# Optimization experiments

Hardware: AMD Instinct MI355X
Metric: run time of the kernel (lower is better)

The kernel has to match this reference:

```python
import jax, jax.numpy as jnp
import numpy as np

NB_HEAD = 8
SIZE_PER_HEAD = 64
MAX_LEN = 1024
D_IN = 512
BATCH = 8
NEG_BIG = 1e12  # matches the torch module's mask * 1000000000000.0


def setup_inputs() -> dict:
    key = jax.random.key(0)
    ks = jax.random.split(key, 6)
    return {
        "Q_seq": jax.random.normal(ks[0], (BATCH, MAX_LEN, D_IN), dtype=jnp.float32),
        "K_seq": jax.random.normal(ks[1], (BATCH, MAX_LEN, D_IN), dtype=jnp.float32),
        "V_seq": jax.random.normal(ks[2], (BATCH, MAX_LEN, D_IN), dtype=jnp.float32),
        "WQ": jax.random.normal(ks[3], (D_IN, NB_HEAD * SIZE_PER_HEAD), dtype=jnp.float32),
        "WK": jax.random.normal(ks[4], (D_IN, NB_HEAD * SIZE_PER_HEAD), dtype=jnp.float32),
        "WV": jax.random.normal(ks[5], (D_IN, NB_HEAD * SIZE_PER_HEAD), dtype=jnp.float32),
    }


def reference(Q_seq, K_seq, V_seq, WQ, WK, WV):
    B, L, _ = Q_seq.shape
    H, D = NB_HEAD, SIZE_PER_HEAD
    # QKV projections -> [B, H, L, D]
    q = (Q_seq @ WQ).reshape(B, L, H, D).transpose(0, 2, 1, 3)
    k = (K_seq @ WK).reshape(B, L, H, D).transpose(0, 2, 1, 3)
    v = (V_seq @ WV).reshape(B, L, H, D).transpose(0, 2, 1, 3)
    # scaled dot-product scores [B, H, Lq, Lk]
    scores = jnp.einsum("bhqd,bhkd->bhqk", q, k) / jnp.sqrt(jnp.float32(D))
    # causal mask: the torch Mask() subtracts 1e12 where key_idx > query_idx
    causal = jnp.triu(jnp.ones((L, L), dtype=scores.dtype), k=1)  # 1 where k > q
    scores = scores - causal[None, None, :, :] * NEG_BIG
    attn = jax.nn.softmax(scores, axis=-1)
    out = jnp.einsum("bhqk,bhkd->bhqd", attn, v)  # [B, H, L, D]
    return out.transpose(0, 2, 1, 3).reshape(B, L, H * D)
```

## Files before the change

### kernel.cpp

```cpp
#include <hip/hip_runtime.h>
#include <cstddef>

#define LEN    1024
#define DIN    512
#define NHEAD  8
#define HDIM   64
#define BATCH  8

typedef __attribute__((ext_vector_type(8))) short  short8;
typedef __attribute__((ext_vector_type(4))) float  f32x4;

#define MFMA16(a, b, c) __builtin_amdgcn_mfma_f32_16x16x32_bf16((a), (b), (c), 0, 0, 0)
#define PERM_HI 0x07060302u
#define PERM_LO 0x05040100u

__device__ __forceinline__ unsigned short bf_hi(float x) {
    unsigned u = __float_as_uint(x);
    return (unsigned short)((u + 0x7fffu + ((u >> 16) & 1u)) >> 16);
}
__device__ __forceinline__ void bf_split(float x, unsigned short& h, unsigned short& l) {
    unsigned u  = __float_as_uint(x);
    unsigned hu = (u + 0x7fffu + ((u >> 16) & 1u)) >> 16;
    h = (unsigned short)hu;
    l = bf_hi(x - __uint_as_float(hu << 16));
}
__device__ __forceinline__ void unpack4(uint4 u, ushort4& h, ushort4& l) {
    h = make_ushort4((unsigned short)(u.x >> 16), (unsigned short)(u.y >> 16),
                     (unsigned short)(u.z >> 16), (unsigned short)(u.w >> 16));
    l = make_ushort4((unsigned short)(u.x & 0xffff), (unsigned short)(u.y & 0xffff),
                     (unsigned short)(u.z & 0xffff), (unsigned short)(u.w & 0xffff));
}
__device__ __forceinline__ void unpack8(uint4 a, uint4 b, uint4& h, uint4& l) {
    h = make_uint4(__builtin_amdgcn_perm(a.y, a.x, PERM_HI),
                   __builtin_amdgcn_perm(a.w, a.z, PERM_HI),
                   __builtin_amdgcn_perm(b.y, b.x, PERM_HI),
                   __builtin_amdgcn_perm(b.w, b.z, PERM_HI));
    l = make_uint4(__builtin_amdgcn_perm(a.y, a.x, PERM_LO),
                   __builtin_amdgcn_perm(a.w, a.z, PERM_LO),
                   __builtin_amdgcn_perm(b.y, b.x, PERM_LO),
                   __builtin_amdgcn_perm(b.w, b.z, PERM_LO));
}

template<int CTRL>
__device__ __forceinline__ float dpp_mov(float x) {
    return __int_as_float(__builtin_amdgcn_update_dpp(
        0, __float_as_int(x), CTRL, 0xF, 0xF, true));
}
__device__ __forceinline__ float red16_max(float x) {
    x = fmaxf(x, dpp_mov<0xB1>(x));
    x = fmaxf(x, dpp_mov<0x4E>(x));
    x = fmaxf(x, dpp_mov<0x141>(x));
    x = fmaxf(x, dpp_mov<0x140>(x));
    return x;
}
__device__ __forceinline__ float red16_sum(float x) {
    x += dpp_mov<0xB1>(x);
    x += dpp_mov<0x4E>(x);
    x += dpp_mov<0x141>(x);
    x += dpp_mov<0x140>(x);
    return x;
}

__global__ __launch_bounds__(256)
void wprep(const float* __restrict__ WQ, const float* __restrict__ WK,
           const float* __restrict__ WV, unsigned short* __restrict__ wt)
{
    __shared__ float T[64][68];
    const int z = blockIdx.z;
    const float* W = (z == 0) ? WQ : (z == 1) ? WK : WV;
    unsigned short* Wth = wt + (size_t)z * 524288;
    unsigned short* Wtl = Wth + 262144;
    const int k0 = blockIdx.x * 64, n0 = blockIdx.y * 64;
    const int t = threadIdx.x;
    #pragma unroll
    for (int e = 0; e < 4; ++e) {
        int f = e * 256 + t, r = f >> 4, c4 = (f & 15) << 2;
        *(float4*)&T[r][c4] = *(const float4*)&W[(size_t)(k0 + r) * 512 + n0 + c4];
    }
    __syncthreads();
    #pragma unroll
    for (int e = 0; e < 4; ++e) {
        int f = e * 256 + t, nr = f >> 4, kc4 = (f & 15) << 2;
        ushort4 h, l;
        bf_split(T[kc4 + 0][nr], h.x, l.x);
        bf_split(T[kc4 + 1][nr], h.y, l.y);
        bf_split(T[kc4 + 2][nr], h.z, l.z);
        bf_split(T[kc4 + 3][nr], h.w, l.w);
        *(ushort4*)&Wth[(size_t)(n0 + nr) * 512 + k0 + kc4] = h;
        *(ushort4*)&Wtl[(size_t)(n0 + nr) * 512 + k0 + kc4] = l;
    }
}

#define PSTR 40

__global__ __launch_bounds__(256, 3)
void proj_mfma(const float* __restrict__ Qin, const float* __restrict__ Kin,
               const float* __restrict__ Vin, const unsigned short* __restrict__ wt,
               unsigned int* __restrict__ qhl, unsigned int* __restrict__ khl,
               unsigned short* __restrict__ vh)
{
    __shared__ unsigned short Ah[128 * PSTR], Al[128 * PSTR],
                              Bh[128 * PSTR], Bl[128 * PSTR];
    const int z = blockIdx.z;
    const bool full = (z < 2);
    const float* X = (z == 0) ? Qin : (z == 1) ? Kin : Vin;
    const unsigned short* Wth = wt + (size_t)z * 524288;
    const unsigned short* Wtl = Wth + 262144;

    const int t = threadIdx.x, lane = t & 63, w = t >> 6;
    const int wm = w & 1, wn = w >> 1;
    const int m0 = blockIdx.x * 128, n0 = blockIdx.y * 128;
    const int lm = lane & 15, lq = lane >> 4;
    const int ar = t >> 1, ak = (t & 1) * 16;

    const float* Xp = X + (size_t)(m0 + ar) * 512 + ak;
    const unsigned short* Bph = Wth + (size_t)(n0 + ar) * 512 + ak;
    const unsigned short* Bpl = Wtl + (size_t)(n0 + ar) * 512 + ak;

    f32x4 acc[4][4];
    #pragma unroll
    for (int i = 0; i < 4; ++i)
        #pragma unroll
        for (int j = 0; j < 4; ++j) acc[i][j] = 0.f;

    float4 av[4];
    uint4 bh0, bh1, bl0, bl1;
    #pragma unroll
    for (int e = 0; e < 4; ++e) av[e] = *(const float4*)(Xp + e * 4);
    bh0 = *(const uint4*)(Bph);
    bh1 = *(const uint4*)(Bph + 8);
    if (full) { bl0 = *(const uint4*)(Bpl); bl1 = *(const uint4*)(Bpl + 8); }

    for (int k0 = 0; k0 < 512; k0 += 32) {
        __syncthreads();
        {
            const float* ff = (const float*)&av[0];
            uint hw[16];
            #pragma unroll
            for (int i = 0; i < 16; ++i) hw[i] = __float_as_uint(ff[i]) & 0xffff0000u;
            uint4 ahv  = make_uint4(__builtin_amdgcn_perm(hw[1],  hw[0],  PERM_HI),
                                    __builtin_amdgcn_perm(hw[3],  hw[2],  PERM_HI),
                                    __builtin_amdgcn_perm(hw[5],  hw[4],  PERM_HI),
                                    __builtin_amdgcn_perm(hw[7],  hw[6],  PERM_HI));
            uint4 ahv2 = make_uint4(__builtin_amdgcn_perm(hw[9],  hw[8],  PERM_HI),
                                    __builtin_amdgcn_perm(hw[11], hw[10], PERM_HI),
                                    __builtin_amdgcn_perm(hw[13], hw[12], PERM_HI),
                                    __builtin_amdgcn_perm(hw[15], hw[14], PERM_HI));
            *(uint4*)&Ah[ar * PSTR + ak]     = ahv;
            *(uint4*)&Ah[ar * PSTR + ak + 8] = ahv2;
            if (full) {
                uint lo[8];
                #pragma unroll
                for (int i = 0; i < 8; ++i) {
                    float r0 = ff[2*i]   - __uint_as_float(hw[2*i]);
                    float r1 = ff[2*i+1] - __uint_as_float(hw[2*i+1]);
                    lo[i] = ((uint)bf_hi(r1) << 16) | bf_hi(r0);
                }
                *(uint4*)&Al[ar * PSTR + ak]     = make_uint4(lo[0], lo[1], lo[2], lo[3]);
                *(uint4*)&Al[ar * PSTR + ak + 8] = make_uint4(lo[4], lo[5], lo[6], lo[7]);
            }
        }
        *(uint4*)&Bh[ar * PSTR + ak]     = bh0;
        *(uint4*)&Bh[ar * PSTR + ak + 8] = bh1;
        if (full) {
            *(uint4*)&Bl[ar * PSTR + ak]     = bl0;
            *(uint4*)&Bl[ar * PSTR + ak + 8] = bl1;
        }
        __syncthreads();

        if (k0 + 32 < 512) {
            #pragma unroll
            for (int e = 0; e < 4; ++e) av[e] = *(const float4*)(Xp + k0 + 32 + e * 4);
            bh0 = *(const uint4*)(Bph + k0 + 32);
            bh1 = *(const uint4*)(Bph + k0 + 40);
            if (full) {
                bl0 = *(const uint4*)(Bpl + k0 + 32);
                bl1 = *(const uint4*)(Bpl + k0 + 40);
            }
        }

        short8 a_h[4], a_l[4];
        #pragma unroll
        for (int mi = 0; mi < 4; ++mi) {
            int off = (wm * 64 + mi * 16 + lm) * PSTR + lq * 8;
            a_h[mi] = *(const short8*)&Ah[off];
            if (full) a_l[mi] = *(const short8*)&Al[off];
        }
        #pragma unroll
        for (int ni = 0; ni < 4; ++ni) {
            int off = (wn * 64 + ni * 16 + lm) * PSTR + lq * 8;
            short8 b_h = *(const short8*)&Bh[off];
            if (full) {
                short8 b_l = *(const short8*)&Bl[off];
                #pragma unroll
                for (int mi = 0; mi < 4; ++mi) {
                    acc[mi][ni] = MFMA16(a_l[mi], b_h, acc[mi][ni]);
                    acc[mi][ni] = MFMA16(a_h[mi], b_l, acc[mi][ni]);
                    acc[mi][ni] = MFMA16(a_h[mi], b_h, acc[mi][ni]);
                }
            } else {
                #pragma unroll
                for (int mi = 0; mi < 4; ++mi)
                    acc[mi][ni] = MFMA16(a_h[mi], b_h, acc[mi][ni]);
            }
        }
    }

    if (z < 2) {
        unsigned int* o = (z == 0) ? qhl : khl;
        const float sc = (z == 0) ? 0.18033688011112042f : 1.0f;
        #pragma unroll
        for (int mi = 0; mi < 4; ++mi)
            #pragma unroll
            for (int ni = 0; ni < 4; ++ni) {
                int n_abs = n0 + wn * 64 + ni * 16 + lm;
                int hd = n_abs >> 6, d = n_abs & 63;
                #pragma unroll
                for (int r = 0; r < 4; ++r) {
                    int m_abs = m0 + wm * 64 + mi * 16 + lq * 4 + r;
                    int b = m_abs >> 10, li = m_abs & 1023;
                    unsigned short hv, lv;
                    bf_split(acc[mi][ni][r] * sc, hv, lv);
                    o[(((size_t)b * NHEAD + hd) * LEN + li) * HDIM + d] =
                        ((unsigned)hv << 16) | lv;
                }
            }
    } else {
        #pragma unroll
        for (int mi = 0; mi < 4; ++mi) {
            int m_base = m0 + wm * 64 + mi * 16 + lq * 4;
            int b = m_base >> 10, l0 = m_base & 1023;
            #pragma unroll
            for (int ni = 0; ni < 4; ++ni) {
                int n_abs = n0 + wn * 64 + ni * 16 + lm;
                int hd = n_abs >> 6, d = n_abs & 63;
                ushort4 hv = make_ushort4(bf_hi(acc[mi][ni][0]), bf_hi(acc[mi][ni][1]),
                                          bf_hi(acc[mi][ni][2]), bf_hi(acc[mi][ni][3]));
                *(ushort4*)&vh[(((size_t)b * NHEAD + hd) * HDIM + d) * LEN + l0] = hv;
            }
        }
    }
}

__global__ __launch_bounds__(256)
void attn_mfma(const unsigned int* __restrict__ qhl, const unsigned int* __restrict__ khl,
               const unsigned short* __restrict__ vth, float* __restrict__ out)
{
    __shared__ unsigned short sm[18432];
    unsigned short* Kh  = sm;
    unsigned short* Kl  = sm + 4608;
    unsigned short* Pb  = sm;
    unsigned short* Vt  = sm + 9728;
    unsigned short* Qsh = sm;
    unsigned short* Qsl = sm + 9216;

    const int t = threadIdx.x, lane = t & 63, w = t >> 6;
    const int lm = lane & 15, lq = lane >> 4;
    const int bx = blockIdx.x;
    const int bh = bx & 63;
    const int g  = (bx >> 6) & 3;
    const int qt = (((bx >> 8) ^ bx) & 1) ? (7 - g) : g;
    const size_t base = (size_t)bh * LEN * HDIM;
    const unsigned int*   qb = qhl + base;
    const unsigned int*   kb = khl + base;
    const unsigned short* vb = vth + base;
    const int Q0  = qt * 128;
    const int Q0w = Q0 + w * 32;

    #pragma unroll
    for (int e = 0; e < 8; ++e) {
        int f = e * 256 + t, r = f >> 4, c4 = (f & 15) << 2;
        uint4 u = *(const uint4*)&qb[(size_t)(Q0 + r) * 64 + c4];
        ushort4 h, l;
        unpack4(u, h, l);
        *(ushort4*)&Qsh[r * 72 + c4] = h;
        *(ushort4*)&Qsl[r * 72 + c4] = l;
    }
    __syncthreads();
    short8 qfh[2][2], qfl[2][2];
    #pragma unroll
    for (int mi = 0; mi < 2; ++mi)
        #pragma unroll
        for (int ks = 0; ks < 2; ++ks) {
            int off = (w * 32 + mi * 16 + lm) * 72 + ks * 32 + lq * 8;
            qfh[mi][ks] = *(const short8*)&Qsh[off];
            qfl[mi][ks] = *(const short8*)&Qsl[off];
        }

    float m_i[2][4], l_i[2][4];
    f32x4 oacc[2][4];
    #pragma unroll
    for (int mi = 0; mi < 2; ++mi)
        #pragma unroll
        for (int r = 0; r < 4; ++r) { m_i[mi][r] = -1e30f; l_i[mi][r] = 0.f; }
    #pragma unroll
    for (int mi = 0; mi < 2; ++mi)
        #pragma unroll
        for (int nd = 0; nd < 4; ++nd) oacc[mi][nd] = 0.f;

    const int kr = t >> 2, kq = t & 3;
    const int vd_ = t >> 3, vs8 = (t & 7) << 3;

    uint4 kreg[4], vreg[2];
    #pragma unroll
    for (int e = 0; e < 4; ++e)
        kreg[e] = *(const uint4*)&kb[(size_t)kr * 64 + kq * 16 + e * 4];
    #pragma unroll
    for (int e = 0; e < 2; ++e)
        vreg[e] = *(const uint4*)&vb[(size_t)(e * 32 + vd_) * LEN + vs8];

    const int jend = 2 * qt + 1;
    for (int jb = 0; jb <= jend; ++jb) {
        __syncthreads();
        {
            uint4 h0, l0, h1, l1;
            unpack8(kreg[0], kreg[1], h0, l0);
            unpack8(kreg[2], kreg[3], h1, l1);
            int ko = kr * 72 + kq * 16;
            *(uint4*)&Kh[ko]     = h0;
            *(uint4*)&Kh[ko + 8] = h1;
            *(uint4*)&Kl[ko]     = l0;
            *(uint4*)&Kl[ko + 8] = l1;
            *(uint4*)&Vt[(vd_)      * 72 + vs8] = vreg[0];
            *(uint4*)&Vt[(vd_ + 32) * 72 + vs8] = vreg[1];
        }
        __syncthreads();

        if (jb < jend) {
            #pragma unroll
            for (int e = 0; e < 4; ++e)
                kreg[e] = *(const uint4*)&kb[(size_t)((jb + 1) * 64 + kr) * 64 + kq * 16 + e * 4];
            #pragma unroll
            for (int e = 0; e < 2; ++e)
                vreg[e] = *(const uint4*)&vb[(size_t)(e * 32 + vd_) * LEN + (jb + 1) * 64 + vs8];
        }

        const bool active = (jb * 64 <= Q0w + 31);
        f32x4 sf[2][4];
        if (active) {
            #pragma unroll
            for (int mi = 0; mi < 2; ++mi)
                #pragma unroll
                for (int ni = 0; ni < 4; ++ni) sf[mi][ni] = 0.f;
            #pragma unroll
            for (int ks = 0; ks < 2; ++ks)
                #pragma unroll
                for (int ni = 0; ni < 4; ++ni) {
                    int off = (ni * 16 + lm) * 72 + ks * 32 + lq * 8;
                    short8 b_h = *(const short8*)&Kh[off];
                    short8 b_l = *(const short8*)&Kl[off];
                    #pragma unroll
                    for (int mi = 0; mi < 2; ++mi) {
                        sf[mi][ni] = MFMA16(qfl[mi][ks], b_h, sf[mi][ni]);
                        sf[mi][ni] = MFMA16(qfh[mi][ks], b_l, sf[mi][ni]);
                        sf[mi][ni] = MFMA16(qfh[mi][ks], b_h, sf[mi][ni]);
                    }
                }
            if (jb * 64 + 63 > Q0w) {
                #pragma unroll
                for (int mi = 0; mi < 2; ++mi)
                    #pragma unroll
                    for (int ni = 0; ni < 4; ++ni) {
                        int key = jb * 64 + ni * 16 + lm;
                        #pragma unroll
                        for (int r = 0; r < 4; ++r) {
                            int qi = Q0w + mi * 16 + lq * 4 + r;
                            if (key > qi) sf[mi][ni][r] = -1e30f;
                        }
                    }
            }
        }
        __syncthreads();

        if (active) {
            #pragma unroll
            for (int mi = 0; mi < 2; ++mi)
                #pragma unroll
                for (int r = 0; r < 4; ++r) {
                    float mv = fmaxf(fmaxf(sf[mi][0][r], sf[mi][1][r]),
                                     fmaxf(sf[mi][2][r], sf[mi][3][r]));
                    mv = red16_max(mv);
                    float mo = m_i[mi][r];
                    float mn = fmaxf(mo, mv);
                    float al = __builtin_amdgcn_exp2f(mo - mn);
                    m_i[mi][r] = mn;
                    float rs = 0.f;
                    int prow = (w * 32 + mi * 16 + lq * 4 + r) * 76 + lm;
                    #pragma unroll
                    for (int ni = 0; ni < 4; ++ni) {
                        float p = __builtin_amdgcn_exp2f(sf[mi][ni][r] - mn);
                        rs += p;
                        Pb[prow + ni * 16] = bf_hi(p);
                    }
                    rs = red16_sum(rs);
                    l_i[mi][r] = l_i[mi][r] * al + rs;
                    #pragma unroll
                    for (int nd = 0; nd < 4; ++nd) oacc[mi][nd][r] *= al;
                }
            short8 pf[2][2];
            #pragma unroll
            for (int mi = 0; mi < 2; ++mi)
                #pragma unroll
                for (int ks = 0; ks < 2; ++ks)
                    pf[mi][ks] = *(const short8*)&Pb[(w * 32 + mi * 16 + lm) * 76 + ks * 32 + lq * 8];
            #pragma unroll
            for (int ks = 0; ks < 2; ++ks)
                #pragma unroll
                for (int nd = 0; nd < 4; ++nd) {
                    short8 vf = *(const short8*)&Vt[(nd * 16 + lm) * 72 + ks * 32 + lq * 8];
                    #pragma unroll
                    for (int mi = 0; mi < 2; ++mi)
                        oacc[mi][nd] = MFMA16(pf[mi][ks], vf, oacc[mi][nd]);
                }
        }
    }

    const int b = bh >> 3, hd = bh & 7;
    #pragma unroll
    for (int mi = 0; mi < 2; ++mi)
        #pragma unroll
        for (int r = 0; r < 4; ++r) {
            int qrow = Q0w + mi * 16 + lq * 4 + r;
            float inv = 1.0f / l_i[mi][r];
            #pragma unroll
            for (int nd = 0; nd < 4; ++nd) {
                int d = nd * 16 + lm;
                out[((size_t)b * LEN + qrow) * (NHEAD * HDIM) + hd * 64 + d] =
                    oacc[mi][nd][r] * inv;
            }
        }
}

extern "C" void kernel_launch(void* const* d_in, const int* in_sizes, int n_in,
                              void* d_out, int out_size, void* d_ws, size_t ws_size,
                              hipStream_t stream)
{
    const float* Qin = (const float*)d_in[0];
    const float* Kin = (const float*)d_in[1];
    const float* Vin = (const float*)d_in[2];
    const float* WQ  = (const float*)d_in[3];
    const float* WK  = (const float*)d_in[4];
    const float* WV  = (const float*)d_in[5];

    const size_t per = (size_t)BATCH * NHEAD * LEN * HDIM;
    unsigned int*   qhl = (unsigned int*)d_ws;
    unsigned int*   khl = qhl + per;
    unsigned short* vh  = (unsigned short*)(khl + per);
    unsigned short* wt  = vh + per;

    wprep    <<<dim3(8, 8, 3),  256, 0, stream>>>(WQ, WK, WV, wt);
    proj_mfma<<<dim3(64, 4, 3), 256, 0, stream>>>(Qin, Kin, Vin, wt, qhl, khl, vh);
    attn_mfma<<<dim3(512),      256, 0, stream>>>(qhl, khl, vh, (float*)d_out);
}
```

Baseline: 188.2 us.

## Widen attention key tile from 64 to 128 and drop per-warp activity gating

Doubles the key/value tile processed per loop iteration in the attention kernel from 64 to 128 keys. This halves the number of iterations and barriers, and loads twice as much K/V per thread per step. The per-warp 'active' skip is removed, so warps whose queries lie entirely before part of the final tile now compute and mask extra scores. Shared memory grows to hold the larger K, V and P tiles, which may lower occupancy.

```diff
diff --git a/kernel.cpp b/kernel.cpp
--- a/kernel.cpp
+++ b/kernel.cpp
@@ -246,11 +246,11 @@
 void attn_mfma(const unsigned int* __restrict__ qhl, const unsigned int* __restrict__ khl,
                const unsigned short* __restrict__ vth, float* __restrict__ out)
 {
-    __shared__ unsigned short sm[18432];
+    __shared__ __align__(16) unsigned short sm[27136];
     unsigned short* Kh  = sm;
-    unsigned short* Kl  = sm + 4608;
+    unsigned short* Kl  = sm + 9216;
     unsigned short* Pb  = sm;
-    unsigned short* Vt  = sm + 9728;
+    unsigned short* Vt  = sm + 18432;
     unsigned short* Qsh = sm;
     unsigned short* Qsl = sm + 9216;
 
@@ -298,120 +298,126 @@
         #pragma unroll
         for (int nd = 0; nd < 4; ++nd) oacc[mi][nd] = 0.f;
 
-    const int kr = t >> 2, kq = t & 3;
-    const int vd_ = t >> 3, vs8 = (t & 7) << 3;
-
-    uint4 kreg[4], vreg[2];
-    #pragma unroll
-    for (int e = 0; e < 4; ++e)
-        kreg[e] = *(const uint4*)&kb[(size_t)kr * 64 + kq * 16 + e * 4];
+    const int kr = t >> 1, kq = t & 1;
+    const int vd_ = t >> 3, vs16 = (t & 7) << 4;
+
+    uint4 kreg[8], vreg[4];
+    #pragma unroll
+    for (int e = 0; e < 8; ++e)
+        kreg[e] = *(const uint4*)&kb[(size_t)kr * 64 + kq * 32 + e * 4];
     #pragma unroll
     for (int e = 0; e < 2; ++e)
-        vreg[e] = *(const uint4*)&vb[(size_t)(e * 32 + vd_) * LEN + vs8];
-
-    const int jend = 2 * qt + 1;
+        #pragma unroll
+        for (int u = 0; u < 2; ++u)
+            vreg[e * 2 + u] = *(const uint4*)&vb[(size_t)(e * 32 + vd_) * LEN + vs16 + u * 8];
+
+    const int jend = qt;
     for (int jb = 0; jb <= jend; ++jb) {
         __syncthreads();
         {
-            uint4 h0, l0, h1, l1;
+            uint4 h0, l0, h1, l1, h2, l2, h3, l3;
             unpack8(kreg[0], kreg[1], h0, l0);
             unpack8(kreg[2], kreg[3], h1, l1);
-            int ko = kr * 72 + kq * 16;
-            *(uint4*)&Kh[ko]     = h0;
-            *(uint4*)&Kh[ko + 8] = h1;
-            *(uint4*)&Kl[ko]     = l0;
-            *(uint4*)&Kl[ko + 8] = l1;
-            *(uint4*)&Vt[(vd_)      * 72 + vs8] = vreg[0];
-            *(uint4*)&Vt[(vd_ + 32) * 72 + vs8] = vreg[1];
+            unpack8(kreg[4], kreg[5], h2, l2);
+            unpack8(kreg[6], kreg[7], h3, l3);
+            int ko = kr * 72 + kq * 32;
+            *(uint4*)&Kh[ko]      = h0;
+            *(uint4*)&Kh[ko + 8]  = h1;
+            *(uint4*)&Kh[ko + 16] = h2;
+            *(uint4*)&Kh[ko + 24] = h3;
+            *(uint4*)&Kl[ko]      = l0;
+            *(uint4*)&Kl[ko + 8]  = l1;
+            *(uint4*)&Kl[ko + 16] = l2;
+            *(uint4*)&Kl[ko + 24] = l3;
+            int vo = vd_ * 136 + vs16;
+            *(uint4*)&Vt[vo]              = vreg[0];
+            *(uint4*)&Vt[vo + 8]          = vreg[1];
+            *(uint4*)&Vt[vo + 32 * 136]     = vreg[2];
+            *(uint4*)&Vt[vo + 32 * 136 + 8] = vreg[3];
         }
         __syncthreads();
 
         if (jb < jend) {
             #pragma unroll
-            for (int e = 0; e < 4; ++e)
-                kreg[e] = *(const uint4*)&kb[(size_t)((jb + 1) * 64 + kr) * 64 + kq * 16 + e * 4];
+            for (int e = 0; e < 8; ++e)
+                kreg[e] = *(const uint4*)&kb[(size_t)((jb + 1) * 128 + kr) * 64 + kq * 32 + e * 4];
             #pragma unroll
             for (int e = 0; e < 2; ++e)
-                vreg[e] = *(const uint4*)&vb[(size_t)(e * 32 + vd_) * LEN + (jb + 1) * 64 + vs8];
-        }
-
-        const bool active = (jb * 64 <= Q0w + 31);
-        f32x4 sf[2][4];
-        if (active) {
+                #pragma unroll
+                for (int u = 0; u < 2; ++u)
+                    vreg[e * 2 + u] = *(const uint4*)&vb[(size_t)(e * 32 + vd_) * LEN + (jb + 1) * 128 + vs16 + u * 8];
+        }
+
+        f32x4 sf[2][8];
+        #pragma unroll
+        for (int mi = 0; mi < 2; ++mi)
+            #pragma unroll
+            for (int ni = 0; ni < 8; ++ni) sf[mi][ni] = 0.f;
+        #pragma unroll
+        for (int ks = 0; ks < 2; ++ks)
+            #pragma unroll
+            for (int ni = 0; ni < 8; ++ni) {
+                int off = (ni * 16 + lm) * 72 + ks * 32 + lq * 8;
+                short8 b_h = *(const short8*)&Kh[off];
+                short8 b_l = *(const short8*)&Kl[off];
+                #pragma unroll
+                for (int mi = 0; mi < 2; ++mi) {
+                    sf[mi][ni] = MFMA16(qfl[mi][ks], b_h, sf[mi][ni]);
+                    sf[mi][ni] = MFMA16(qfh[mi][ks], b_l, sf[mi][ni]);
+                    sf[mi][ni] = MFMA16(qfh[mi][ks], b_h, sf[mi][ni]);
+                }
+            }
+        if (jb == jend) {
             #pragma unroll
             for (int mi = 0; mi < 2; ++mi)
                 #pragma unroll
-                for (int ni = 0; ni < 4; ++ni) sf[mi][ni] = 0.f;
-            #pragma unroll
-            for (int ks = 0; ks < 2; ++ks)
-                #pragma unroll
-                for (int ni = 0; ni < 4; ++ni) {
-                    int off = (ni * 16 + lm) * 72 + ks * 32 + lq * 8;
-                    short8 b_h = *(const short8*)&Kh[off];
-                    short8 b_l = *(const short8*)&Kl[off];
+                for (int ni = 0; ni < 8; ++ni) {
+                    int key = jb * 128 + ni * 16 + lm;
                     #pragma unroll
-                    for (int mi = 0; mi < 2; ++mi) {
-                        sf[mi][ni] = MFMA16(qfl[mi][ks], b_h, sf[mi][ni]);
-                        sf[mi][ni] = MFMA16(qfh[mi][ks], b_l, sf[mi][ni]);
-                        sf[mi][ni] = MFMA16(qfh[mi][ks], b_h, sf[mi][ni]);
+                    for (int r = 0; r < 4; ++r) {
+                        int qi = Q0w + mi * 16 + lq * 4 + r;
+                        if (key > qi) sf[mi][ni][r] = -1e30f;
                     }
                 }
-            if (jb * 64 + 63 > Q0w) {
-                #pragma unroll
-                for (int mi = 0; mi < 2; ++mi)
-                    #pragma unroll
-                    for (int ni = 0; ni < 4; ++ni) {
-                        int key = jb * 64 + ni * 16 + lm;
-                        #pragma unroll
-                        for (int r = 0; r < 4; ++r) {
-                            int qi = Q0w + mi * 16 + lq * 4 + r;
-                            if (key > qi) sf[mi][ni][r] = -1e30f;
-                        }
-                    }
-            }
         }
         __syncthreads();
 
-        if (active) {
-            #pragma unroll
-            for (int mi = 0; mi < 2; ++mi)
-                #pragma unroll
-                for (int r = 0; r < 4; ++r) {
-                    float mv = fmaxf(fmaxf(sf[mi][0][r], sf[mi][1][r]),
-                                     fmaxf(sf[mi][2][r], sf[mi][3][r]));
-                    mv = red16_max(mv);
-                    float mo = m_i[mi][r];
-                    float mn = fmaxf(mo, mv);
-                    float al = __builtin_amdgcn_exp2f(mo - mn);
-                    m_i[mi][r] = mn;
-                    float rs = 0.f;
-                    int prow = (w * 32 + mi * 16 + lq * 4 + r) * 76 + lm;
-                    #pragma unroll
-                    for (int ni = 0; ni < 4; ++ni) {
-                        float p = __builtin_amdgcn_exp2f(sf[mi][ni][r] - mn);
-                        rs += p;
-                        Pb[prow + ni * 16] = bf_hi(p);
-                    }
-                    rs = red16_sum(rs);
-                    l_i[mi][r] = l_i[mi][r] * al + rs;
-                    #pragma unroll
-                    for (int nd = 0; nd < 4; ++nd) oacc[mi][nd][r] *= al;
-                }
-            short8 pf[2][2];
-            #pragma unroll
-            for (int mi = 0; mi < 2; ++mi)
-                #pragma unroll
-                for (int ks = 0; ks < 2; ++ks)
-                    pf[mi][ks] = *(const short8*)&Pb[(w * 32 + mi * 16 + lm) * 76 + ks * 32 + lq * 8];
-            #pragma unroll
-            for (int ks = 0; ks < 2; ++ks)
-                #pragma unroll
-                for (int nd = 0; nd < 4; ++nd) {
-                    short8 vf = *(const short8*)&Vt[(nd * 16 + lm) * 72 + ks * 32 + lq * 8];
-                    #pragma unroll
-                    for (int mi = 0; mi < 2; ++mi)
-                        oacc[mi][nd] = MFMA16(pf[mi][ks], vf, oacc[mi][nd]);
-                }
+        #pragma unroll
+        for (int mi = 0; mi < 2; ++mi)
+            #pragma unroll
+            for (int r = 0; r < 4; ++r) {
+                float mv = fmaxf(fmaxf(fmaxf(sf[mi][0][r], sf[mi][1][r]),
+                                       fmaxf(sf[mi][2][r], sf[mi][3][r])),
+                                 fmaxf(fmaxf(sf[mi][4][r], sf[mi][5][r]),
+                                       fmaxf(sf[mi][6][r], sf[mi][7][r])));
+                mv = red16_max(mv);
+                float mo = m_i[mi][r];
+                float mn = fmaxf(mo, mv);
+                float al = __builtin_amdgcn_exp2f(mo - mn);
+                m_i[mi][r] = mn;
+                float rs = 0.f;
+                int prow = (w * 32 + mi * 16 + lq * 4 + r) * 132 + lm;
+                #pragma unroll
+                for (int ni = 0; ni < 8; ++ni) {
+                    float p = __builtin_amdgcn_exp2f(sf[mi][ni][r] - mn);
+                    rs += p;
+                    Pb[prow + ni * 16] = bf_hi(p);
+                }
+                rs = red16_sum(rs);
+                l_i[mi][r] = l_i[mi][r] * al + rs;
+                #pragma unroll
+                for (int nd = 0; nd < 4; ++nd) oacc[mi][nd][r] *= al;
+            }
+        #pragma unroll
+        for (int ks = 0; ks < 4; ++ks) {
+            short8 pf0 = *(const short8*)&Pb[(w * 32 + 0  + lm) * 132 + ks * 32 + lq * 8];
+            short8 pf1 = *(const short8*)&Pb[(w * 32 + 16 + lm) * 132 + ks * 32 + lq * 8];
+            #pragma unroll
+            for (int nd = 0; nd < 4; ++nd) {
+                short8 vf = *(const short8*)&Vt[(nd * 16 + lm) * 136 + ks * 32 + lq * 8];
+                oacc[0][nd] = MFMA16(pf0, vf, oacc[0][nd]);
+                oacc[1][nd] = MFMA16(pf1, vf, oacc[1][nd]);
+            }
         }
     }
 
```

New measurement: 204.6 us. +8.7%, slower.

## Split attention KV range across two blocks and merge with a combine kernel

Applied to the files above, without the earlier changes.

The attention kernel now splits each query tile's key/value blocks into even and odd halves, so 1024 blocks run instead of 512. Each block writes unnormalized partial outputs plus running max and sum to workspace, and a new combine kernel merges the two halves and normalizes. The goal is more parallelism to fill the GPU's CUs, and it drops the previous causal load-balancing remap. The cost is an extra kernel launch and a round trip of partial results through global memory. The combine step uses exp2 on the stored max values, which assumes the partial kernel keeps m in log2 scale.

```diff
diff --git a/kernel.cpp b/kernel.cpp
--- a/kernel.cpp
+++ b/kernel.cpp
@@ -242,9 +242,10 @@
     }
 }
 
-__global__ __launch_bounds__(256)
-void attn_mfma(const unsigned int* __restrict__ qhl, const unsigned int* __restrict__ khl,
-               const unsigned short* __restrict__ vth, float* __restrict__ out)
+__global__ __launch_bounds__(256, 4)
+void attn_part(const unsigned int* __restrict__ qhl, const unsigned int* __restrict__ khl,
+               const unsigned short* __restrict__ vth,
+               float* __restrict__ opart, float* __restrict__ mlpart)
 {
     __shared__ unsigned short sm[18432];
     unsigned short* Kh  = sm;
@@ -258,8 +259,8 @@
     const int lm = lane & 15, lq = lane >> 4;
     const int bx = blockIdx.x;
     const int bh = bx & 63;
-    const int g  = (bx >> 6) & 3;
-    const int qt = (((bx >> 8) ^ bx) & 1) ? (7 - g) : g;
+    const int h  = (bx >> 6) & 1;
+    const int qt = (bx >> 7) & 7;
     const size_t base = (size_t)bh * LEN * HDIM;
     const unsigned int*   qb = qhl + base;
     const unsigned int*   kb = khl + base;
@@ -271,10 +272,10 @@
     for (int e = 0; e < 8; ++e) {
         int f = e * 256 + t, r = f >> 4, c4 = (f & 15) << 2;
         uint4 u = *(const uint4*)&qb[(size_t)(Q0 + r) * 64 + c4];
-        ushort4 h, l;
-        unpack4(u, h, l);
-        *(ushort4*)&Qsh[r * 72 + c4] = h;
-        *(ushort4*)&Qsl[r * 72 + c4] = l;
+        ushort4 hh, ll;
+        unpack4(u, hh, ll);
+        *(ushort4*)&Qsh[r * 72 + c4] = hh;
+        *(ushort4*)&Qsl[r * 72 + c4] = ll;
     }
     __syncthreads();
     short8 qfh[2][2], qfl[2][2];
@@ -304,13 +305,13 @@
     uint4 kreg[4], vreg[2];
     #pragma unroll
     for (int e = 0; e < 4; ++e)
-        kreg[e] = *(const uint4*)&kb[(size_t)kr * 64 + kq * 16 + e * 4];
+        kreg[e] = *(const uint4*)&kb[(size_t)(h * 64 + kr) * 64 + kq * 16 + e * 4];
     #pragma unroll
     for (int e = 0; e < 2; ++e)
-        vreg[e] = *(const uint4*)&vb[(size_t)(e * 32 + vd_) * LEN + vs8];
+        vreg[e] = *(const uint4*)&vb[(size_t)(e * 32 + vd_) * LEN + h * 64 + vs8];
 
     const int jend = 2 * qt + 1;
-    for (int jb = 0; jb <= jend; ++jb) {
+    for (int jb = h; jb <= jend; jb += 2) {
         __syncthreads();
         {
             uint4 h0, l0, h1, l1;
@@ -326,13 +327,13 @@
         }
         __syncthreads();
 
-        if (jb < jend) {
+        if (jb + 2 <= jend) {
             #pragma unroll
             for (int e = 0; e < 4; ++e)
-                kreg[e] = *(const uint4*)&kb[(size_t)((jb + 1) * 64 + kr) * 64 + kq * 16 + e * 4];
+                kreg[e] = *(const uint4*)&kb[(size_t)((jb + 2) * 64 + kr) * 64 + kq * 16 + e * 4];
             #pragma unroll
             for (int e = 0; e < 2; ++e)
-                vreg[e] = *(const uint4*)&vb[(size_t)(e * 32 + vd_) * LEN + (jb + 1) * 64 + vs8];
+                vreg[e] = *(const uint4*)&vb[(size_t)(e * 32 + vd_) * LEN + (jb + 2) * 64 + vs8];
         }
 
         const bool active = (jb * 64 <= Q0w + 31);
@@ -415,20 +416,52 @@
         }
     }
 
-    const int b = bh >> 3, hd = bh & 7;
+    float* op  = opart  + ((size_t)h * 64 + bh) * (LEN * HDIM);
+    float* mlp = mlpart + ((size_t)h * 64 + bh) * (LEN * 2);
     #pragma unroll
     for (int mi = 0; mi < 2; ++mi)
         #pragma unroll
         for (int r = 0; r < 4; ++r) {
             int qrow = Q0w + mi * 16 + lq * 4 + r;
-            float inv = 1.0f / l_i[mi][r];
             #pragma unroll
             for (int nd = 0; nd < 4; ++nd) {
                 int d = nd * 16 + lm;
-                out[((size_t)b * LEN + qrow) * (NHEAD * HDIM) + hd * 64 + d] =
-                    oacc[mi][nd][r] * inv;
-            }
-        }
+                op[(size_t)qrow * HDIM + d] = oacc[mi][nd][r];
+            }
+            if (lm == 0) {
+                mlp[qrow * 2]     = m_i[mi][r];
+                mlp[qrow * 2 + 1] = l_i[mi][r];
+            }
+        }
+}
+
+__global__ __launch_bounds__(256)
+void attn_combine(const float* __restrict__ opart, const float* __restrict__ mlpart,
+                  float* __restrict__ out)
+{
+    int gid = blockIdx.x * 256 + threadIdx.x;
+    int c4  = (gid & 15) * 4;
+    int row = (gid >> 4) & 1023;
+    int bh  = gid >> 14;
+    size_t o0 = ((size_t)bh * LEN + row) * HDIM + c4;
+    size_t o1 = o0 + (size_t)64 * LEN * HDIM;
+    const float* ml0 = mlpart + ((size_t)bh * LEN + row) * 2;
+    const float* ml1 = ml0 + (size_t)64 * LEN * 2;
+    float m0 = ml0[0], l0 = ml0[1];
+    float m1 = ml1[0], l1 = ml1[1];
+    float M  = fmaxf(m0, m1);
+    float w0 = __builtin_amdgcn_exp2f(m0 - M);
+    float w1 = __builtin_amdgcn_exp2f(m1 - M);
+    float inv = 1.0f / (l0 * w0 + l1 * w1);
+    float4 a = *(const float4*)&opart[o0];
+    float4 b = *(const float4*)&opart[o1];
+    float4 r;
+    r.x = (a.x * w0 + b.x * w1) * inv;
+    r.y = (a.y * w0 + b.y * w1) * inv;
+    r.z = (a.z * w0 + b.z * w1) * inv;
+    r.w = (a.w * w0 + b.w * w1) * inv;
+    int bb = bh >> 3, hd = bh & 7;
+    *(float4*)&out[((size_t)bb * LEN + row) * (NHEAD * HDIM) + hd * 64 + c4] = r;
 }
 
 extern "C" void kernel_launch(void* const* d_in, const int* in_sizes, int n_in,
@@ -447,8 +480,11 @@
     unsigned int*   khl = qhl + per;
     unsigned short* vh  = (unsigned short*)(khl + per);
     unsigned short* wt  = vh + per;
-
-    wprep    <<<dim3(8, 8, 3),  256, 0, stream>>>(WQ, WK, WV, wt);
-    proj_mfma<<<dim3(64, 4, 3), 256, 0, stream>>>(Qin, Kin, Vin, wt, qhl, khl, vh);
-    attn_mfma<<<dim3(512),      256, 0, stream>>>(qhl, khl, vh, (float*)d_out);
-}
+    float* opart  = (float*)(wt + (size_t)3 * 524288);
+    float* mlpart = opart + (size_t)2 * 64 * LEN * HDIM;
+
+    wprep       <<<dim3(8, 8, 3),  256, 0, stream>>>(WQ, WK, WV, wt);
+    proj_mfma   <<<dim3(64, 4, 3), 256, 0, stream>>>(Qin, Kin, Vin, wt, qhl, khl, vh);
+    attn_part   <<<dim3(1024),     256, 0, stream>>>(qhl, khl, vh, opart, mlpart);
+    attn_combine<<<dim3(4096),     256, 0, stream>>>(opart, mlpart, (float*)d_out);
+}
```

Measured after the change: 246.6 us. 1.31x slower.
